# Performance work log

Measured on AMD Instinct MI355X. Metric: run time of the kernel, lower is better.

## Reference

```python
import jax, jax.numpy as jnp
import numpy as np

B, T, C, WE, H2 = 64, 256, 2048, 256, 1024  # batch, seq_len, num_classes, we_dim, 2*encoder_hidden_size


def setup_inputs() -> dict:
    key = jax.random.key(0)
    ks = jax.random.split(key, 8)
    s = 0.02
    encoder_outputs = jax.random.normal(ks[0], (B, T, H2), jnp.float32)
    words_num = jax.random.randint(ks[1], (B,), T // 2, T + 1)
    mask = jnp.arange(T)[None, :] < words_num[:, None]  # True = valid position
    targets = jax.random.randint(ks[2], (B, T), 0, C, dtype=jnp.int32)
    E = jax.random.normal(ks[3], (C, WE), jnp.float32) * s          # decoder token embedding
    W_ih = jax.random.normal(ks[4], (3 * H2, WE), jnp.float32) * s  # GRU input weights (r,z,n)
    W_hh = jax.random.normal(ks[5], (3 * H2, H2), jnp.float32) * s  # GRU hidden weights (r,z,n)
    b_ih = jnp.zeros((3 * H2,), jnp.float32)
    b_hh = jnp.zeros((3 * H2,), jnp.float32)
    W_out = jax.random.normal(ks[6], (C, 2 * H2), jnp.float32) * s  # Linear(4*enc_hidden -> C)
    b_out = jnp.zeros((C,), jnp.float32)
    return dict(encoder_outputs=encoder_outputs, mask=mask, targets=targets,
                E=E, W_ih=W_ih, W_hh=W_hh, b_ih=b_ih, b_hh=b_hh,
                W_out=W_out, b_out=b_out)


def reference(encoder_outputs, mask, targets, E, W_ih, W_hh, b_ih, b_hh, W_out, b_out):
    Bb, Tt, H = encoder_outputs.shape
    # Decoder hidden init: last encoder timestep (num_layers=1)
    h0 = encoder_outputs[:, -1, :]  # [B, H]
    # Teacher forcing: step-0 input is token id 0 (torch.zeros long), then targets[:, :-1]
    ids = jnp.concatenate([jnp.zeros((Bb, 1), targets.dtype), targets[:, :-1]], axis=1)
    x_seq = jnp.swapaxes(E[ids], 0, 1)  # [T, B, WE]
    # Precompute all GRU input projections in one GEMM: [T, B, 3H]
    gi = jnp.einsum('tbe,ge->tbg', x_seq, W_ih) + b_ih

    def step(h, gi_t):
        gh = h @ W_hh.T + b_hh                       # [B, 3H]
        ir, iz, inn = jnp.split(gi_t, 3, axis=-1)
        hr, hz, hn = jnp.split(gh, 3, axis=-1)
        r = jax.nn.sigmoid(ir + hr)
        z = jax.nn.sigmoid(iz + hz)
        n = jnp.tanh(inn + r * hn)
        h_new = (1.0 - z) * n + z * h                # GRU output == new hidden (1 step)
        # Luong dot attention: query = GRU output, keys = encoder outputs
        e = jnp.einsum('bh,bth->bt', h_new, encoder_outputs)
        e = jnp.where(mask, e, -jnp.inf)             # e[~valid] = -inf
        alpha = jax.nn.softmax(e, axis=-1)
        c = jnp.einsum('bt,bth->bh', alpha, encoder_outputs)
        logits = jnp.concatenate([h_new, c], axis=-1) @ W_out.T + b_out  # [B, C]
        return h_new, logits

    _, outs = jax.lax.scan(step, h0, gi)             # outs: [T, B, C]
    return jnp.swapaxes(outs, 0, 1)                  # [B, T, C]
```

## Files before the change

kernel.cpp:

```cpp
#include <hip/hip_runtime.h>
#include <hip/hip_bf16.h>
#include <math.h>

#define B_ 64
#define T_ 256
#define C_ 2048
#define WE_ 256
#define H_ 1024
#define G3_ 3072

typedef __attribute__((ext_vector_type(8))) short short8;
typedef __attribute__((ext_vector_type(4))) float f32x4;

__device__ __forceinline__ float sigmoidf_(float x) { return 1.f / (1.f + expf(-x)); }

__device__ __forceinline__ unsigned short f2bf(float v) {
    union { float f; unsigned int u; } x; x.f = v;
    unsigned int r = x.u + 0x7fffu + ((x.u >> 16) & 1u);
    return (unsigned short)(r >> 16);
}
__device__ __forceinline__ float bf2f(unsigned short h) {
    union { unsigned int u; float f; } x; x.u = ((unsigned int)h) << 16;
    return x.f;
}


__global__ void k_maskprep(const unsigned char* __restrict__ m, float* __restrict__ mf) {
    int idx = blockIdx.x * 256 + threadIdx.x;
    bool bytemode = (m[1] != 0);
    unsigned char v = bytemode ? m[idx] : m[(size_t)idx * 4];
    mf[idx] = v ? 1.f : 0.f;
}


__global__ void k_hinit2(const float* __restrict__ enc, float* __restrict__ h32,
                         unsigned short* __restrict__ h0h, unsigned short* __restrict__ h0l) {
    int idx = blockIdx.x * 256 + threadIdx.x;
    int b = idx >> 10, k = idx & (H_ - 1);
    float v = enc[((size_t)b * T_ + (T_ - 1)) * H_ + k];
    h32[idx] = v;
    unsigned short hi = f2bf(v);
    h0h[idx] = hi;
    h0l[idx] = f2bf(v - bf2f(hi));
}

__global__ void k_wgprep(const float* __restrict__ Wih, const float* __restrict__ Whh,
                         unsigned short* __restrict__ Wgh, unsigned short* __restrict__ Wgl) {
    int row = blockIdx.x;
    int c4 = threadIdx.x;
    int col = c4 * 4;
    float4 v = (col < 256) ? *(const float4*)&Wih[(size_t)row * 256 + col]
                           : *(const float4*)&Whh[(size_t)row * 1024 + col - 256];
    unsigned short h[4], l[4];
    float vv[4] = {v.x, v.y, v.z, v.w};
#pragma unroll
    for (int i = 0; i < 4; ++i) { h[i] = f2bf(vv[i]); l[i] = f2bf(vv[i] - bf2f(h[i])); }
    size_t o = (size_t)row * 1280 + col;
    *(uint2*)&Wgh[o] = *(const uint2*)h;
    *(uint2*)&Wgl[o] = *(const uint2*)l;
}

__global__ void k_xemb(const float* __restrict__ E, const int* __restrict__ targets,
                       unsigned short* __restrict__ Xeh, unsigned short* __restrict__ Xel) {
    int t = blockIdx.x, b = blockIdx.y, l = threadIdx.x;
    int id = (t == 0) ? 0 : targets[b * T_ + t - 1];
    float4 v = *(const float4*)&E[(size_t)id * 256 + l * 4];
    unsigned short h[4], lo[4];
    float vv[4] = {v.x, v.y, v.z, v.w};
#pragma unroll
    for (int i = 0; i < 4; ++i) { h[i] = f2bf(vv[i]); lo[i] = f2bf(vv[i] - bf2f(h[i])); }
    size_t o = (size_t)t * 16384 + (size_t)b * 256 + l * 4;
    *(uint2*)&Xeh[o] = *(const uint2*)h;
    *(uint2*)&Xel[o] = *(const uint2*)lo;
}

__global__ void k_encprep(const float* __restrict__ enc,
                          unsigned short* __restrict__ ench, unsigned short* __restrict__ encl) {
    size_t i4 = (size_t)blockIdx.x * 256 + threadIdx.x;
    float4 v = *(const float4*)&enc[i4 * 4];
    unsigned short h[4], l[4];
    float vv[4] = {v.x, v.y, v.z, v.w};
#pragma unroll
    for (int i = 0; i < 4; ++i) { h[i] = f2bf(vv[i]); l[i] = f2bf(vv[i] - bf2f(h[i])); }
    *(uint2*)&ench[i4 * 4] = *(const uint2*)h;
    *(uint2*)&encl[i4 * 4] = *(const uint2*)l;
}

__global__ __launch_bounds__(256) void k_step(
    const unsigned short* __restrict__ Xeh_t, const unsigned short* __restrict__ Xel_t,
    const unsigned short* __restrict__ Aph, const unsigned short* __restrict__ Apl, int ap_stride,
    const unsigned short* __restrict__ Wgh, const unsigned short* __restrict__ Wgl,
    const float* __restrict__ bih, const float* __restrict__ bhh,
    const float* __restrict__ h_prev32, float* __restrict__ h_next32,
    unsigned short* __restrict__ HhO, unsigned short* __restrict__ HlO)
{
    __shared__ unsigned short Ah[64 * 40], Al[64 * 40], Bh[48 * 40], Bl[48 * 40];
    __shared__ float bR[16], bZ[16], bNX[16], bNH[16];
    const int tid = threadIdx.x;
    const int j0 = blockIdx.x * 16;
    const int wave = tid >> 6, lane = tid & 63;
    const int ml = lane & 15, quad = lane >> 4;
    if (tid < 16) {
        int j = j0 + tid;
        bR[tid] = bih[j] + bhh[j];
        bZ[tid] = bih[1024 + j] + bhh[1024 + j];
        bNX[tid] = bih[2048 + j];
        bNH[tid] = bhh[2048 + j];
    }
    f32x4 accR = {0,0,0,0}, accZ = {0,0,0,0}, accNX = {0,0,0,0}, accNH = {0,0,0,0};
    const int ar = tid >> 2, aq = tid & 3;
    uint4 rAh = {0,0,0,0}, rAl = {0,0,0,0}, rBh = {0,0,0,0}, rBl = {0,0,0,0};
    {
        size_t off = (size_t)ar * 256 + aq * 8;
        rAh = *(const uint4*)&Xeh_t[off];
        rAl = *(const uint4*)&Xel_t[off];
    }
    if (tid < 192) {
        int g = ar >> 4, jj = ar & 15;
        size_t off = (size_t)(g * 1024 + j0 + jj) * 1280 + aq * 8;
        rBh = *(const uint4*)&Wgh[off];
        rBl = *(const uint4*)&Wgl[off];
    }
    for (int c = 0; c < 40; ++c) {
        *(uint4*)&Ah[ar * 40 + aq * 8] = rAh;
        *(uint4*)&Al[ar * 40 + aq * 8] = rAl;
        if (tid < 192) {
            *(uint4*)&Bh[ar * 40 + aq * 8] = rBh;
            *(uint4*)&Bl[ar * 40 + aq * 8] = rBl;
        }
        __syncthreads();
        if (c + 1 < 40) {
            int k0 = (c + 1) * 32;
            if (k0 < 256) {
                size_t off = (size_t)ar * 256 + k0 + aq * 8;
                rAh = *(const uint4*)&Xeh_t[off];
                rAl = *(const uint4*)&Xel_t[off];
            } else {
                size_t off = (size_t)ar * ap_stride + (k0 - 256) + aq * 8;
                rAh = *(const uint4*)&Aph[off];
                rAl = *(const uint4*)&Apl[off];
            }
            if (tid < 192) {
                int g = ar >> 4, jj = ar & 15;
                size_t off = (size_t)(g * 1024 + j0 + jj) * 1280 + k0 + aq * 8;
                rBh = *(const uint4*)&Wgh[off];
                rBl = *(const uint4*)&Wgl[off];
            }
        }
        short8 ah = *(const short8*)&Ah[(wave * 16 + ml) * 40 + quad * 8];
        short8 al = *(const short8*)&Al[(wave * 16 + ml) * 40 + quad * 8];
        short8 bh0 = *(const short8*)&Bh[(0 * 16 + ml) * 40 + quad * 8];
        short8 bl0 = *(const short8*)&Bl[(0 * 16 + ml) * 40 + quad * 8];
        short8 bh1 = *(const short8*)&Bh[(1 * 16 + ml) * 40 + quad * 8];
        short8 bl1 = *(const short8*)&Bl[(1 * 16 + ml) * 40 + quad * 8];
        short8 bh2 = *(const short8*)&Bh[(2 * 16 + ml) * 40 + quad * 8];
        short8 bl2 = *(const short8*)&Bl[(2 * 16 + ml) * 40 + quad * 8];
        accR = __builtin_amdgcn_mfma_f32_16x16x32_bf16(ah, bh0, accR, 0, 0, 0);
        accR = __builtin_amdgcn_mfma_f32_16x16x32_bf16(ah, bl0, accR, 0, 0, 0);
        accR = __builtin_amdgcn_mfma_f32_16x16x32_bf16(al, bh0, accR, 0, 0, 0);
        accZ = __builtin_amdgcn_mfma_f32_16x16x32_bf16(ah, bh1, accZ, 0, 0, 0);
        accZ = __builtin_amdgcn_mfma_f32_16x16x32_bf16(ah, bl1, accZ, 0, 0, 0);
        accZ = __builtin_amdgcn_mfma_f32_16x16x32_bf16(al, bh1, accZ, 0, 0, 0);
        if (c < 8) {
            accNX = __builtin_amdgcn_mfma_f32_16x16x32_bf16(ah, bh2, accNX, 0, 0, 0);
            accNX = __builtin_amdgcn_mfma_f32_16x16x32_bf16(ah, bl2, accNX, 0, 0, 0);
            accNX = __builtin_amdgcn_mfma_f32_16x16x32_bf16(al, bh2, accNX, 0, 0, 0);
        } else {
            accNH = __builtin_amdgcn_mfma_f32_16x16x32_bf16(ah, bh2, accNH, 0, 0, 0);
            accNH = __builtin_amdgcn_mfma_f32_16x16x32_bf16(ah, bl2, accNH, 0, 0, 0);
            accNH = __builtin_amdgcn_mfma_f32_16x16x32_bf16(al, bh2, accNH, 0, 0, 0);
        }
        __syncthreads();
    }
    int j = j0 + ml;
    float brv = bR[ml], bzv = bZ[ml], bnxv = bNX[ml], bnhv = bNH[ml];
#pragma unroll
    for (int reg = 0; reg < 4; ++reg) {
        int b = wave * 16 + quad * 4 + reg;
        float r = sigmoidf_(accR[reg] + brv);
        float z = sigmoidf_(accZ[reg] + bzv);
        float n = tanhf((accNX[reg] + bnxv) + r * (accNH[reg] + bnhv));
        float hp = h_prev32[(size_t)b * 1024 + j];
        float hv = (1.f - z) * n + z * hp;
        h_next32[(size_t)b * 1024 + j] = hv;
        unsigned short hi = f2bf(hv);
        HhO[(size_t)b * 262144 + j] = hi;
        HlO[(size_t)b * 262144 + j] = f2bf(hv - bf2f(hi));
    }
}

__global__ __launch_bounds__(256) void k_scoresK(
    const unsigned short* __restrict__ Hh, const unsigned short* __restrict__ Hl,
    const unsigned short* __restrict__ ench, const unsigned short* __restrict__ encl,
    float* __restrict__ e_all)
{
    __shared__ unsigned short Ahs[128 * 40], Als[128 * 40], Bhs[128 * 40], Bls[128 * 40];
    const int tid = threadIdx.x;
    const int b = blockIdx.y;
    const int t0 = (blockIdx.x & 1) * 128, p0 = (blockIdx.x >> 1) * 128;
    const int lane = tid & 63, wave = tid >> 6;
    const int wm = (wave & 1) * 64, wn = (wave >> 1) * 64;
    const int ml = lane & 15, quad = lane >> 4;
    const unsigned short* Ahp = Hh + (size_t)b * 262144;
    const unsigned short* Alp = Hl + (size_t)b * 262144;
    const unsigned short* Bhp = ench + (size_t)b * 262144;
    const unsigned short* Blp = encl + (size_t)b * 262144;
    f32x4 acc[4][4];
#pragma unroll
    for (int a = 0; a < 4; ++a)
#pragma unroll
        for (int c = 0; c < 4; ++c) acc[a][c] = (f32x4){0.f, 0.f, 0.f, 0.f};

    for (int kc = 0; kc < 32; ++kc) {
#pragma unroll
        for (int r2 = 0; r2 < 2; ++r2) {
            int s = tid + 256 * r2;
            int row = s >> 2, q = s & 3;
            size_t ga = (size_t)(t0 + row) * 1024 + kc * 32 + q * 8;
            size_t gb = (size_t)(p0 + row) * 1024 + kc * 32 + q * 8;
            *(uint4*)&Ahs[row * 40 + q * 8] = *(const uint4*)&Ahp[ga];
            *(uint4*)&Als[row * 40 + q * 8] = *(const uint4*)&Alp[ga];
            *(uint4*)&Bhs[row * 40 + q * 8] = *(const uint4*)&Bhp[gb];
            *(uint4*)&Bls[row * 40 + q * 8] = *(const uint4*)&Blp[gb];
        }
        __syncthreads();
        short8 ah[4], al[4], bh[4], bl[4];
#pragma unroll
        for (int mt = 0; mt < 4; ++mt) {
            ah[mt] = *(const short8*)&Ahs[(wm + mt * 16 + ml) * 40 + quad * 8];
            al[mt] = *(const short8*)&Als[(wm + mt * 16 + ml) * 40 + quad * 8];
        }
#pragma unroll
        for (int nt = 0; nt < 4; ++nt) {
            bh[nt] = *(const short8*)&Bhs[(wn + nt * 16 + ml) * 40 + quad * 8];
            bl[nt] = *(const short8*)&Bls[(wn + nt * 16 + ml) * 40 + quad * 8];
        }
#pragma unroll
        for (int mt = 0; mt < 4; ++mt)
#pragma unroll
            for (int nt = 0; nt < 4; ++nt) {
                acc[mt][nt] = __builtin_amdgcn_mfma_f32_16x16x32_bf16(ah[mt], bh[nt], acc[mt][nt], 0, 0, 0);
                acc[mt][nt] = __builtin_amdgcn_mfma_f32_16x16x32_bf16(ah[mt], bl[nt], acc[mt][nt], 0, 0, 0);
                acc[mt][nt] = __builtin_amdgcn_mfma_f32_16x16x32_bf16(al[mt], bh[nt], acc[mt][nt], 0, 0, 0);
            }
        __syncthreads();
    }
#pragma unroll
    for (int mt = 0; mt < 4; ++mt)
#pragma unroll
        for (int nt = 0; nt < 4; ++nt)
#pragma unroll
            for (int reg = 0; reg < 4; ++reg) {
                int t = t0 + wm + mt * 16 + quad * 4 + reg;
                int p = p0 + wn + nt * 16 + ml;
                e_all[((size_t)b * 256 + t) * 256 + p] = acc[mt][nt][reg];
            }
}

__global__ __launch_bounds__(256) void k_softmaxK(
    const float* __restrict__ e_all, const float* __restrict__ maskf,
    unsigned short* __restrict__ Ab)
{
    const int tid = threadIdx.x;
    const int ridx = blockIdx.x * 4 + (tid >> 6);
    const int lane = tid & 63;
    const int b = ridx >> 8, t = ridx & 255;
    const float* er = e_all + ((size_t)b * 256 + t) * 256;
    const float* mr = maskf + (size_t)b * 256;
    float v[4];
#pragma unroll
    for (int i = 0; i < 4; ++i) {
        int p = lane + 64 * i;
        v[i] = (mr[p] > 0.5f) ? er[p] : -INFINITY;
    }
    float m = fmaxf(fmaxf(v[0], v[1]), fmaxf(v[2], v[3]));
#pragma unroll
    for (int off = 32; off > 0; off >>= 1) m = fmaxf(m, __shfl_xor(m, off));
    float s = 0.f;
#pragma unroll
    for (int i = 0; i < 4; ++i) { v[i] = expf(v[i] - m); s += v[i]; }
#pragma unroll
    for (int off = 32; off > 0; off >>= 1) s += __shfl_xor(s, off);
    float inv = 1.f / s;
    unsigned short* arr = Ab + ((size_t)b * 256 + t) * 256;
#pragma unroll
    for (int i = 0; i < 4; ++i) arr[lane + 64 * i] = f2bf(v[i] * inv);
}

__global__ __launch_bounds__(256) void k_contextK(
    const unsigned short* __restrict__ Ab, const unsigned short* __restrict__ ench,
    unsigned short* __restrict__ Cb)
{
    __shared__ unsigned short As[128 * 40];
    __shared__ unsigned short Bs[128 * 40];
    const int tid = threadIdx.x;
    const int b = blockIdx.y;
    const int t0 = (blockIdx.x & 1) * 128;
    const int k0 = (blockIdx.x >> 1) * 128;
    const int lane = tid & 63, wave = tid >> 6;
    const int wm = (wave & 1) * 64, wn = (wave >> 1) * 64;
    const int ml = lane & 15, quad = lane >> 4;
    f32x4 acc[4][4];
#pragma unroll
    for (int a = 0; a < 4; ++a)
#pragma unroll
        for (int c = 0; c < 4; ++c) acc[a][c] = (f32x4){0.f, 0.f, 0.f, 0.f};

    for (int c = 0; c < 8; ++c) {
#pragma unroll
        for (int r2 = 0; r2 < 2; ++r2) {
            int s = tid + 256 * r2;
            int row = s >> 2, q = s & 3;
            *(uint4*)&As[row * 40 + q * 8] =
                *(const uint4*)&Ab[((size_t)b * 256 + t0 + row) * 256 + c * 32 + q * 8];
        }
        {
            int tr = tid >> 3, kq = tid & 7;
            const unsigned short* src =
                ench + ((size_t)b * 256 + c * 32 + tr) * 1024 + k0 + kq * 16;
            unsigned short tmp[16];
            *(uint4*)&tmp[0] = *(const uint4*)&src[0];
            *(uint4*)&tmp[8] = *(const uint4*)&src[8];
#pragma unroll
            for (int i = 0; i < 16; ++i)
                Bs[(kq * 16 + i) * 40 + tr] = tmp[i];
        }
        __syncthreads();
        short8 af[4], bf[4];
#pragma unroll
        for (int mt = 0; mt < 4; ++mt)
            af[mt] = *(const short8*)&As[(wm + mt * 16 + ml) * 40 + quad * 8];
#pragma unroll
        for (int nt = 0; nt < 4; ++nt)
            bf[nt] = *(const short8*)&Bs[(wn + nt * 16 + ml) * 40 + quad * 8];
#pragma unroll
        for (int mt = 0; mt < 4; ++mt)
#pragma unroll
            for (int nt = 0; nt < 4; ++nt)
                acc[mt][nt] = __builtin_amdgcn_mfma_f32_16x16x32_bf16(af[mt], bf[nt], acc[mt][nt], 0, 0, 0);
        __syncthreads();
    }
#pragma unroll
    for (int mt = 0; mt < 4; ++mt)
#pragma unroll
        for (int nt = 0; nt < 4; ++nt)
#pragma unroll
            for (int reg = 0; reg < 4; ++reg) {
                int t = t0 + wm + mt * 16 + quad * 4 + reg;
                int k = k0 + wn + nt * 16 + ml;
                Cb[((size_t)b * 256 + t) * 1024 + k] = f2bf(acc[mt][nt][reg]);
            }
}

__global__ __launch_bounds__(256) void k_finalK(
    const unsigned short* __restrict__ Hh, const unsigned short* __restrict__ Cb,
    const unsigned short* __restrict__ Wb,
    const float* __restrict__ bout, float* __restrict__ out)
{
    __shared__ unsigned short As[128 * 40];
    __shared__ unsigned short Bs[128 * 40];
    const int tid = threadIdx.x;
    const int gr0 = blockIdx.x * 128;
    const int j0  = blockIdx.y * 128;
    const int lane = tid & 63, wave = tid >> 6;
    const int wm = (wave & 1) * 64, wn = (wave >> 1) * 64;
    const int ml = lane & 15, quad = lane >> 4;
    f32x4 acc[4][4];
#pragma unroll
    for (int a = 0; a < 4; ++a)
#pragma unroll
        for (int c = 0; c < 4; ++c) acc[a][c] = (f32x4){0.f, 0.f, 0.f, 0.f};

    for (int kc = 0; kc < 64; ++kc) {
        const unsigned short* asrc = (kc < 32) ? Hh : Cb;
        int ko = (kc & 31) * 32;
#pragma unroll
        for (int r2 = 0; r2 < 2; ++r2) {
            int s = tid + 256 * r2;
            int row = s >> 2, q = s & 3;
            *(uint4*)&As[row * 40 + q * 8] =
                *(const uint4*)&asrc[(size_t)(gr0 + row) * 1024 + ko + q * 8];
            *(uint4*)&Bs[row * 40 + q * 8] =
                *(const uint4*)&Wb[(size_t)(j0 + row) * 2048 + kc * 32 + q * 8];
        }
        __syncthreads();
        short8 af[4], bf[4];
#pragma unroll
        for (int mt = 0; mt < 4; ++mt)
            af[mt] = *(const short8*)&As[(wm + mt * 16 + ml) * 40 + quad * 8];
#pragma unroll
        for (int nt = 0; nt < 4; ++nt)
            bf[nt] = *(const short8*)&Bs[(wn + nt * 16 + ml) * 40 + quad * 8];
#pragma unroll
        for (int mt = 0; mt < 4; ++mt)
#pragma unroll
            for (int nt = 0; nt < 4; ++nt)
                acc[mt][nt] = __builtin_amdgcn_mfma_f32_16x16x32_bf16(af[mt], bf[nt], acc[mt][nt], 0, 0, 0);
        __syncthreads();
    }
#pragma unroll
    for (int nt = 0; nt < 4; ++nt) {
        int j = j0 + wn + nt * 16 + ml;
        float bo = bout[j];
#pragma unroll
        for (int mt = 0; mt < 4; ++mt)
#pragma unroll
            for (int reg = 0; reg < 4; ++reg) {
                int r = gr0 + wm + mt * 16 + quad * 4 + reg;
                out[(size_t)r * 2048 + j] = acc[mt][nt][reg] + bo;
            }
    }
}


__global__ void k_hinit(const float* __restrict__ enc, float* __restrict__ h) {
    int idx = blockIdx.x * 256 + threadIdx.x;
    int b = idx >> 10, k = idx & (H_ - 1);
    h[idx] = enc[((size_t)b * T_ + (T_ - 1)) * H_ + k];
}

__global__ void k_wprep(const float* __restrict__ Wout, __hip_bfloat16* __restrict__ Wb) {
    int i4 = blockIdx.x * 256 + threadIdx.x;
    float4 v = *(const float4*)&Wout[(size_t)i4 * 4];
    __attribute__((aligned(8))) __hip_bfloat16 tmp[4] = {
        __float2bfloat16(v.x), __float2bfloat16(v.y),
        __float2bfloat16(v.z), __float2bfloat16(v.w)};
    *(uint2*)&Wb[(size_t)i4 * 4] = *(const uint2*)tmp;
}

__global__ __launch_bounds__(256) void k_gates(
    const float* __restrict__ E, const int* __restrict__ targets,
    const float* __restrict__ Wih, const float* __restrict__ Whh,
    const float* __restrict__ bih, const float* __restrict__ bhh,
    const float* __restrict__ h_cur,
    float* __restrict__ gi, float* __restrict__ gh0, float* __restrict__ gh1,
    int t)
{
    __shared__ float As[32 * 68];
    __shared__ float Ws[32 * 34];
    __shared__ int ids[B_];
    const int tid = threadIdx.x;
    const int z = blockIdx.y;
    const int j0 = blockIdx.x * 32;
    const int tx = tid & 15;
    const int ty = tid >> 4;
    float accI[4][2], accH[4][2];
#pragma unroll
    for (int i = 0; i < 4; ++i) { accI[i][0]=0.f; accI[i][1]=0.f; accH[i][0]=0.f; accH[i][1]=0.f; }
    if (tid < B_) ids[tid] = (t == 0) ? 0 : targets[tid * T_ + t - 1];
    __syncthreads();
    if (z == 0) {
        for (int c = 0; c < 8; ++c) {
            int k0 = c * 32;
#pragma unroll
            for (int r = 0; r < 2; ++r) {
                int lin = tid + 256 * r;
                int k4 = lin & 7, b = lin >> 3;
                float4 v = *(const float4*)&E[(size_t)ids[b] * WE_ + k0 + k4 * 4];
                int kk = k4 * 4;
                As[(kk + 0) * 68 + b] = v.x; As[(kk + 1) * 68 + b] = v.y;
                As[(kk + 2) * 68 + b] = v.z; As[(kk + 3) * 68 + b] = v.w;
            }
            {
                int k4 = tid & 7, jj = tid >> 3;
                float4 v = *(const float4*)&Wih[(size_t)(j0 + jj) * WE_ + k0 + k4 * 4];
                int kk = k4 * 4;
                Ws[(kk + 0) * 34 + jj] = v.x; Ws[(kk + 1) * 34 + jj] = v.y;
                Ws[(kk + 2) * 34 + jj] = v.z; Ws[(kk + 3) * 34 + jj] = v.w;
            }
            __syncthreads();
#pragma unroll
            for (int kk = 0; kk < 32; ++kk) {
                float4 a = *(const float4*)&As[kk * 68 + ty * 4];
                float2 w = *(const float2*)&Ws[kk * 34 + tx * 2];
                accI[0][0] += a.x * w.x; accI[0][1] += a.x * w.y;
                accI[1][0] += a.y * w.x; accI[1][1] += a.y * w.y;
                accI[2][0] += a.z * w.x; accI[2][1] += a.z * w.y;
                accI[3][0] += a.w * w.x; accI[3][1] += a.w * w.y;
            }
            __syncthreads();
        }
    }
    const int c_lo = (z == 0) ? 0 : 12;
    const int c_hi = (z == 0) ? 12 : 32;
    for (int c = c_lo; c < c_hi; ++c) {
        int k0 = c * 32;
#pragma unroll
        for (int r = 0; r < 2; ++r) {
            int lin = tid + 256 * r;
            int k4 = lin & 7, b = lin >> 3;
            float4 v = *(const float4*)&h_cur[(size_t)b * H_ + k0 + k4 * 4];
            int kk = k4 * 4;
            As[(kk + 0) * 68 + b] = v.x; As[(kk + 1) * 68 + b] = v.y;
            As[(kk + 2) * 68 + b] = v.z; As[(kk + 3) * 68 + b] = v.w;
        }
        {
            int k4 = tid & 7, jj = tid >> 3;
            float4 v = *(const float4*)&Whh[(size_t)(j0 + jj) * H_ + k0 + k4 * 4];
            int kk = k4 * 4;
            Ws[(kk + 0) * 34 + jj] = v.x; Ws[(kk + 1) * 34 + jj] = v.y;
            Ws[(kk + 2) * 34 + jj] = v.z; Ws[(kk + 3) * 34 + jj] = v.w;
        }
        __syncthreads();
#pragma unroll
        for (int kk = 0; kk < 32; ++kk) {
            float4 a = *(const float4*)&As[kk * 68 + ty * 4];
            float2 w = *(const float2*)&Ws[kk * 34 + tx * 2];
            accH[0][0] += a.x * w.x; accH[0][1] += a.x * w.y;
            accH[1][0] += a.y * w.x; accH[1][1] += a.y * w.y;
            accH[2][0] += a.z * w.x; accH[2][1] += a.z * w.y;
            accH[3][0] += a.w * w.x; accH[3][1] += a.w * w.y;
        }
        __syncthreads();
    }
#pragma unroll
    for (int p = 0; p < 2; ++p) {
        int j = j0 + tx * 2 + p;
        if (z == 0) {
            float vi = bih[j], vh = bhh[j];
#pragma unroll
            for (int i = 0; i < 4; ++i) {
                int b = ty * 4 + i;
                gi[(size_t)b * G3_ + j]  = accI[i][p] + vi;
                gh0[(size_t)b * G3_ + j] = accH[i][p] + vh;
            }
        } else {
#pragma unroll
            for (int i = 0; i < 4; ++i) {
                int b = ty * 4 + i;
                gh1[(size_t)b * G3_ + j] = accH[i][p];
            }
        }
    }
}

__global__ __launch_bounds__(256) void k_score_h(
    const float* __restrict__ gi, const float* __restrict__ gh0, const float* __restrict__ gh1,
    const float* __restrict__ h_prev, const float* __restrict__ enc,
    float* __restrict__ e_raw, float* __restrict__ h_next,
    __hip_bfloat16* __restrict__ Xb, int t, int use_x)
{
    __shared__ float hs[H_];
    const int b = blockIdx.y;
    const int tc = blockIdx.x;
    const int tid = threadIdx.x;
#pragma unroll
    for (int i = 0; i < 4; ++i) {
        int k = i * 256 + tid;
        size_t o = (size_t)b * G3_ + k;
        float ir = gi[o], iz = gi[o + H_], in = gi[o + 2 * H_];
        float hr = gh0[o] + gh1[o];
        float hz = gh0[o + H_] + gh1[o + H_];
        float hn = gh0[o + 2 * H_] + gh1[o + 2 * H_];
        float r = sigmoidf_(ir + hr);
        float z = sigmoidf_(iz + hz);
        float n = tanhf(in + r * hn);
        float hv = (1.f - z) * n + z * h_prev[(size_t)b * H_ + k];
        hs[k] = hv;
        if (tc == 0) {
            h_next[(size_t)b * H_ + k] = hv;
            if (use_x) Xb[((size_t)b * T_ + t) * C_ + k] = __float2bfloat16(hv);
        }
    }
    __syncthreads();
    const int tl = tid >> 2, part = tid & 3;
    const int tt = tc * 64 + tl;
    const float4* row = (const float4*)(enc + ((size_t)b * T_ + tt) * H_);
    const float4* hv4 = (const float4*)hs;
    float acc = 0.f;
#pragma unroll 8
    for (int i = 0; i < 64; ++i) {
        float4 a = row[part * 64 + i];
        float4 x = hv4[part * 64 + i];
        acc += a.x * x.x + a.y * x.y + a.z * x.z + a.w * x.w;
    }
    acc += __shfl_xor(acc, 1);
    acc += __shfl_xor(acc, 2);
    if (part == 0) e_raw[(size_t)b * T_ + tt] = acc;
}

__global__ __launch_bounds__(256) void k_ctx(
    const float* __restrict__ e_raw, const float* __restrict__ maskf,
    const float* __restrict__ enc, float* __restrict__ cvec,
    __hip_bfloat16* __restrict__ Xb, int t, int use_x)
{
    __shared__ float al[T_];
    __shared__ float red[256];
    const int b = blockIdx.y, q = blockIdx.x, tid = threadIdx.x;
    float e = (maskf[(size_t)b * T_ + tid] > 0.5f) ? e_raw[(size_t)b * T_ + tid] : -INFINITY;
    red[tid] = e; __syncthreads();
    for (int s = 128; s > 0; s >>= 1) { if (tid < s) red[tid] = fmaxf(red[tid], red[tid + s]); __syncthreads(); }
    float mx = red[0]; __syncthreads();
    float p = expf(e - mx);
    red[tid] = p; __syncthreads();
    for (int s = 128; s > 0; s >>= 1) { if (tid < s) red[tid] += red[tid + s]; __syncthreads(); }
    float denom = red[0];
    al[tid] = p / denom;
    __syncthreads();
    const int k = q * 256 + tid;
    float acc = 0.f;
#pragma unroll 8
    for (int tt2 = 0; tt2 < T_; ++tt2) {
        acc += al[tt2] * enc[((size_t)b * T_ + tt2) * H_ + k];
    }
    if (use_x) Xb[((size_t)b * T_ + t) * C_ + H_ + k] = __float2bfloat16(acc);
    else       cvec[(size_t)b * H_ + k] = acc;
}

__global__ __launch_bounds__(256) void k_logits(
    const float* __restrict__ h, const float* __restrict__ cvec,
    const float* __restrict__ Wout, const float* __restrict__ bout,
    float* __restrict__ out, int t)
{
    __shared__ float As[32 * 68];
    __shared__ float Ws[32 * 33];
    const int tid = threadIdx.x;
    const int j0 = blockIdx.x * 32;
    const int tx = tid & 31;
    const int ty = tid >> 5;
    float acc[8];
#pragma unroll
    for (int i = 0; i < 8; ++i) acc[i] = 0.f;
    for (int c = 0; c < 64; ++c) {
        int k0 = c * 32;
        const float* Ap = (k0 < H_) ? (h + k0) : (cvec + (k0 - H_));
#pragma unroll
        for (int r = 0; r < 2; ++r) {
            int lin = tid + 256 * r;
            int k4 = lin & 7, b = lin >> 3;
            float4 v = *(const float4*)&Ap[(size_t)b * H_ + k4 * 4];
            int kk = k4 * 4;
            As[(kk + 0) * 68 + b] = v.x; As[(kk + 1) * 68 + b] = v.y;
            As[(kk + 2) * 68 + b] = v.z; As[(kk + 3) * 68 + b] = v.w;
        }
        {
            int k4 = tid & 7, jj = tid >> 3;
            float4 v = *(const float4*)&Wout[(size_t)(j0 + jj) * (2 * H_) + k0 + k4 * 4];
            int kk = k4 * 4;
            Ws[(kk + 0) * 33 + jj] = v.x; Ws[(kk + 1) * 33 + jj] = v.y;
            Ws[(kk + 2) * 33 + jj] = v.z; Ws[(kk + 3) * 33 + jj] = v.w;
        }
        __syncthreads();
#pragma unroll
        for (int kk = 0; kk < 32; ++kk) {
            float w = Ws[kk * 33 + tx];
#pragma unroll
            for (int i = 0; i < 8; ++i) acc[i] += As[kk * 68 + ty * 8 + i] * w;
        }
        __syncthreads();
    }
    float bo = bout[j0 + tx];
#pragma unroll
    for (int i = 0; i < 8; ++i) {
        int b = ty * 8 + i;
        out[((size_t)b * T_ + t) * C_ + j0 + tx] = acc[i] + bo;
    }
}

__global__ __launch_bounds__(256) void k_final(
    const __hip_bfloat16* __restrict__ Xb, const __hip_bfloat16* __restrict__ Wb,
    const float* __restrict__ bout, float* __restrict__ out)
{
    __shared__ __hip_bfloat16 As[128 * 40];
    __shared__ __hip_bfloat16 Bs[128 * 40];
    const int tid = threadIdx.x;
    const int gr0 = blockIdx.x * 128;
    const int j0  = blockIdx.y * 128;
    const int lane = tid & 63, wave = tid >> 6;
    const int wm = (wave & 1) * 64, wn = (wave >> 1) * 64;
    const int ml = lane & 15, quad = lane >> 4;
    f32x4 acc[4][4];
#pragma unroll
    for (int a = 0; a < 4; ++a)
#pragma unroll
        for (int b = 0; b < 4; ++b) acc[a][b] = (f32x4){0.f, 0.f, 0.f, 0.f};
    for (int kc = 0; kc < 64; ++kc) {
#pragma unroll
        for (int r = 0; r < 2; ++r) {
            int s = tid + 256 * r;
            int row = s >> 2, kq = s & 3;
            *(uint4*)&As[row * 40 + kq * 8] =
                *(const uint4*)&Xb[(size_t)(gr0 + row) * 2048 + kc * 32 + kq * 8];
            *(uint4*)&Bs[row * 40 + kq * 8] =
                *(const uint4*)&Wb[(size_t)(j0 + row) * 2048 + kc * 32 + kq * 8];
        }
        __syncthreads();
        short8 af[4], bf[4];
#pragma unroll
        for (int mt = 0; mt < 4; ++mt)
            af[mt] = *(const short8*)&As[(wm + mt * 16 + ml) * 40 + quad * 8];
#pragma unroll
        for (int nt = 0; nt < 4; ++nt)
            bf[nt] = *(const short8*)&Bs[(wn + nt * 16 + ml) * 40 + quad * 8];
#pragma unroll
        for (int mt = 0; mt < 4; ++mt)
#pragma unroll
            for (int nt = 0; nt < 4; ++nt)
                acc[mt][nt] = __builtin_amdgcn_mfma_f32_16x16x32_bf16(af[mt], bf[nt], acc[mt][nt], 0, 0, 0);
        __syncthreads();
    }
#pragma unroll
    for (int nt = 0; nt < 4; ++nt) {
        int j = j0 + wn + nt * 16 + ml;
        float bo = bout[j];
#pragma unroll
        for (int mt = 0; mt < 4; ++mt) {
#pragma unroll
            for (int reg = 0; reg < 4; ++reg) {
                int r = gr0 + wm + mt * 16 + quad * 4 + reg;
                out[(size_t)r * 2048 + j] = acc[mt][nt][reg] + bo;
            }
        }
    }
}


extern "C" void kernel_launch(void* const* d_in, const int* in_sizes, int n_in,
                              void* d_out, int out_size, void* d_ws, size_t ws_size,
                              hipStream_t stream)
{
    const float* enc     = (const float*)d_in[0];
    const unsigned char* mask = (const unsigned char*)d_in[1];
    const int*   targets = (const int*)d_in[2];
    const float* E       = (const float*)d_in[3];
    const float* Wih     = (const float*)d_in[4];
    const float* Whh     = (const float*)d_in[5];
    const float* bih     = (const float*)d_in[6];
    const float* bhh     = (const float*)d_in[7];
    const float* Wout    = (const float*)d_in[8];
    const float* bout    = (const float*)d_in[9];
    float* out = (float*)d_out;

    const size_t NEED_FULL = 235000000ull;
    const size_t NEED_MID  = 819200ull * 4 + (4194304ull + 33554432ull) * 2;

    if (ws_size >= NEED_FULL) {
        char* p = (char*)d_ws;
        float* h32a = (float*)p;              p += 262144;
        float* h32b = (float*)p;              p += 262144;
        unsigned short* h0h = (unsigned short*)p; p += 131072;
        unsigned short* h0l = (unsigned short*)p; p += 131072;
        float* maskf = (float*)p;             p += 65536;
        unsigned short* Wgh = (unsigned short*)p; p += 7864320;
        unsigned short* Wgl = (unsigned short*)p; p += 7864320;
        unsigned short* Xeh = (unsigned short*)p; p += 8388608;
        unsigned short* Xel = (unsigned short*)p; p += 8388608;
        unsigned short* ench = (unsigned short*)p; p += 33554432;
        unsigned short* encl = (unsigned short*)p; p += 33554432;
        unsigned short* Hh = (unsigned short*)p;  p += 33554432;
        unsigned short* Hl = (unsigned short*)p;  p += 33554432;
        float* e_all = (float*)p;             p += 16777216;
        unsigned short* Ab = (unsigned short*)p;  p += 8388608;
        unsigned short* Cb = (unsigned short*)p;  p += 33554432;
        unsigned short* Wb = (unsigned short*)p;  p += 8388608;

        k_maskprep<<<64, 256, 0, stream>>>(mask, maskf);
        k_hinit2<<<256, 256, 0, stream>>>(enc, h32a, h0h, h0l);
        k_wgprep<<<3072, 320, 0, stream>>>(Wih, Whh, Wgh, Wgl);
        k_xemb<<<dim3(256, 64), 64, 0, stream>>>(E, targets, Xeh, Xel);
        k_encprep<<<16384, 256, 0, stream>>>(enc, ench, encl);
        k_wprep<<<4096, 256, 0, stream>>>(Wout, (__hip_bfloat16*)Wb);

        for (int t = 0; t < T_; ++t) {
            const unsigned short* Xeh_t = Xeh + (size_t)t * 16384;
            const unsigned short* Xel_t = Xel + (size_t)t * 16384;
            const unsigned short* Aph = (t == 0) ? h0h : (Hh + (size_t)(t - 1) * 1024);
            const unsigned short* Apl = (t == 0) ? h0l : (Hl + (size_t)(t - 1) * 1024);
            int ap_stride = (t == 0) ? 1024 : 262144;
            const float* hp = (t & 1) ? h32b : h32a;
            float* hn = (t & 1) ? h32a : h32b;
            k_step<<<64, 256, 0, stream>>>(Xeh_t, Xel_t, Aph, Apl, ap_stride,
                                           Wgh, Wgl, bih, bhh, hp, hn,
                                           Hh + (size_t)t * 1024, Hl + (size_t)t * 1024);
        }
        k_scoresK<<<dim3(4, 64), 256, 0, stream>>>(Hh, Hl, ench, encl, e_all);
        k_softmaxK<<<4096, 256, 0, stream>>>(e_all, maskf, Ab);
        k_contextK<<<dim3(16, 64), 256, 0, stream>>>(Ab, ench, Cb);
        k_finalK<<<dim3(128, 16), 256, 0, stream>>>(Hh, Cb, Wb, bout, out);
        return;
    }

    float* ws    = (float*)d_ws;
    float* hbuf  = ws;
    float* gi    = ws + 131072;
    float* gh0   = gi + 196608;
    float* gh1   = gh0 + 196608;
    float* e_raw = gh1 + 196608;
    float* maskf = e_raw + 16384;
    float* cvec  = maskf + 16384;
    __hip_bfloat16* Wb = (__hip_bfloat16*)(ws + 819200);
    __hip_bfloat16* Xb = Wb + 4194304;

    const int fast = (ws_size >= NEED_MID) ? 1 : 0;

    k_maskprep<<<64, 256, 0, stream>>>(mask, maskf);
    k_hinit<<<256, 256, 0, stream>>>(enc, hbuf);
    if (fast) k_wprep<<<4096, 256, 0, stream>>>(Wout, Wb);

    for (int t = 0; t < T_; ++t) {
        float* h_cur  = hbuf + (t & 1) * 65536;
        float* h_next = hbuf + ((t + 1) & 1) * 65536;
        k_gates<<<dim3(96, 2), 256, 0, stream>>>(E, targets, Wih, Whh, bih, bhh,
                                                 h_cur, gi, gh0, gh1, t);
        k_score_h<<<dim3(4, 64), 256, 0, stream>>>(gi, gh0, gh1, h_cur, enc,
                                                   e_raw, h_next, Xb, t, fast);
        k_ctx<<<dim3(4, 64), 256, 0, stream>>>(e_raw, maskf, enc, cvec, Xb, t, fast);
        if (!fast)
            k_logits<<<64, 256, 0, stream>>>(h_next, cvec, Wout, bout, out, t);
    }
    if (fast)
        k_final<<<dim3(128, 16), 256, 0, stream>>>(Xb, Wb, bout, out);
}
```

Baseline: 6.162 ms.

## Replace per-timestep GRU launches with persistent kernel using grid-wide barrier

Swaps the 256 per-step k_step launches for a single persistent k_rnn kernel of 128 blocks. The blocks synchronize through a global atomic counter barrier, and split-K partial sums pass between paired blocks via flags and a global scratch buffer. Weights are read straight from global memory (L2) into registers with software prefetch instead of being staged through LDS. This removes launch overhead and per-step LDS staging, at the cost of spin-wait barriers. It also relies on all 128 blocks being co-resident, or the barrier will deadlock.

```diff
diff --git a/kernel.cpp b/kernel.cpp
--- a/kernel.cpp
+++ b/kernel.cpp
@@ -24,6 +24,12 @@
     return x.f;
 }
 
+#define LD8(p, off) (*(const short8*)((p) + (off)))
+
+
+__global__ void k_zero(unsigned int* __restrict__ p) {
+    p[blockIdx.x * 256 + threadIdx.x] = 0u;
+}
 
 __global__ void k_maskprep(const unsigned char* __restrict__ m, float* __restrict__ mf) {
     int idx = blockIdx.x * 256 + threadIdx.x;
@@ -32,16 +38,14 @@
     mf[idx] = v ? 1.f : 0.f;
 }
 
-
-__global__ void k_hinit2(const float* __restrict__ enc, float* __restrict__ h32,
-                         unsigned short* __restrict__ h0h, unsigned short* __restrict__ h0l) {
+__global__ void k_hinit0(const float* __restrict__ enc,
+                         unsigned short* __restrict__ Hh, unsigned short* __restrict__ Hl) {
     int idx = blockIdx.x * 256 + threadIdx.x;
-    int b = idx >> 10, k = idx & (H_ - 1);
+    int b = idx >> 10, k = idx & 1023;
     float v = enc[((size_t)b * T_ + (T_ - 1)) * H_ + k];
-    h32[idx] = v;
     unsigned short hi = f2bf(v);
-    h0h[idx] = hi;
-    h0l[idx] = f2bf(v - bf2f(hi));
+    Hh[idx] = hi;
+    Hl[idx] = f2bf(v - bf2f(hi));
 }
 
 __global__ void k_wgprep(const float* __restrict__ Wih, const float* __restrict__ Whh,
@@ -86,108 +90,167 @@
     *(uint2*)&encl[i4 * 4] = *(const uint2*)l;
 }
 
-__global__ __launch_bounds__(256) void k_step(
-    const unsigned short* __restrict__ Xeh_t, const unsigned short* __restrict__ Xel_t,
-    const unsigned short* __restrict__ Aph, const unsigned short* __restrict__ Apl, int ap_stride,
+__global__ void k_wprep(const float* __restrict__ Wout, unsigned short* __restrict__ Wb) {
+    int i4 = blockIdx.x * 256 + threadIdx.x;
+    float4 v = *(const float4*)&Wout[(size_t)i4 * 4];
+    unsigned short t[4] = {f2bf(v.x), f2bf(v.y), f2bf(v.z), f2bf(v.w)};
+    *(uint2*)&Wb[(size_t)i4 * 4] = *(const uint2*)t;
+}
+
+__global__ __launch_bounds__(512, 2) void k_rnn(
+    const unsigned short* __restrict__ Xeh, const unsigned short* __restrict__ Xel,
     const unsigned short* __restrict__ Wgh, const unsigned short* __restrict__ Wgl,
     const float* __restrict__ bih, const float* __restrict__ bhh,
-    const float* __restrict__ h_prev32, float* __restrict__ h_next32,
-    unsigned short* __restrict__ HhO, unsigned short* __restrict__ HlO)
-{
-    __shared__ unsigned short Ah[64 * 40], Al[64 * 40], Bh[48 * 40], Bl[48 * 40];
-    __shared__ float bR[16], bZ[16], bNX[16], bNH[16];
+    unsigned short* __restrict__ Hh, unsigned short* __restrict__ Hl,
+    float* __restrict__ gpart, unsigned int* __restrict__ flags,
+    unsigned int* __restrict__ barcnt)
+{
+    __shared__ float red[3072];
     const int tid = threadIdx.x;
-    const int j0 = blockIdx.x * 16;
     const int wave = tid >> 6, lane = tid & 63;
     const int ml = lane & 15, quad = lane >> 4;
-    if (tid < 16) {
-        int j = j0 + tid;
-        bR[tid] = bih[j] + bhh[j];
-        bZ[tid] = bih[1024 + j] + bhh[1024 + j];
-        bNX[tid] = bih[2048 + j];
-        bNH[tid] = bhh[2048 + j];
-    }
-    f32x4 accR = {0,0,0,0}, accZ = {0,0,0,0}, accNX = {0,0,0,0}, accNH = {0,0,0,0};
-    const int ar = tid >> 2, aq = tid & 3;
-    uint4 rAh = {0,0,0,0}, rAl = {0,0,0,0}, rBh = {0,0,0,0}, rBl = {0,0,0,0};
-    {
-        size_t off = (size_t)ar * 256 + aq * 8;
-        rAh = *(const uint4*)&Xeh_t[off];
-        rAl = *(const uint4*)&Xel_t[off];
-    }
-    if (tid < 192) {
-        int g = ar >> 4, jj = ar & 15;
-        size_t off = (size_t)(g * 1024 + j0 + jj) * 1280 + aq * 8;
-        rBh = *(const uint4*)&Wgh[off];
-        rBl = *(const uint4*)&Wgl[off];
-    }
-    for (int c = 0; c < 40; ++c) {
-        *(uint4*)&Ah[ar * 40 + aq * 8] = rAh;
-        *(uint4*)&Al[ar * 40 + aq * 8] = rAl;
-        if (tid < 192) {
-            *(uint4*)&Bh[ar * 40 + aq * 8] = rBh;
-            *(uint4*)&Bl[ar * 40 + aq * 8] = rBl;
-        }
-        __syncthreads();
-        if (c + 1 < 40) {
-            int k0 = (c + 1) * 32;
-            if (k0 < 256) {
-                size_t off = (size_t)ar * 256 + k0 + aq * 8;
-                rAh = *(const uint4*)&Xeh_t[off];
-                rAl = *(const uint4*)&Xel_t[off];
+    const int mw = wave & 3, ksub = wave >> 2;
+    const int triple = blockIdx.x >> 1, kh = blockIdx.x & 1;
+    const int j0 = triple * 16;
+    const int m0 = mw * 16;
+    const int kbase = kh * 640 + ksub * 320;
+
+    float bRv = 0.f, bZv = 0.f, bNXv = 0.f, bNHv = 0.f;
+    if (kh == 0 && ksub == 0) {
+        int j = j0 + ml;
+        bRv = bih[j] + bhh[j];
+        bZv = bih[1024 + j] + bhh[1024 + j];
+        bNXv = bih[2048 + j];
+        bNHv = bhh[2048 + j];
+    }
+
+    const size_t bo = (size_t)(j0 + ml) * 1280 + quad * 8;
+    const unsigned short* BrH = Wgh + bo;
+    const unsigned short* BrL = Wgl + bo;
+    const unsigned short* BzH = Wgh + bo + (size_t)1024 * 1280;
+    const unsigned short* BzL = Wgl + bo + (size_t)1024 * 1280;
+    const unsigned short* BnH = Wgh + bo + (size_t)2048 * 1280;
+    const unsigned short* BnL = Wgl + bo + (size_t)2048 * 1280;
+
+    const unsigned short* AxH = Xeh + (size_t)(m0 + ml) * 256 + quad * 8;
+    const unsigned short* AxL = Xel + (size_t)(m0 + ml) * 256 + quad * 8;
+    const unsigned short* AhH = Hh + (size_t)(m0 + ml) * 1024 + quad * 8 - 256;
+    const unsigned short* AhL = Hl + (size_t)(m0 + ml) * 1024 + quad * 8 - 256;
+    const unsigned short* Hh_t = Hh;
+    const unsigned short* Hl_t = Hl;
+
+    for (int t = 0; t < 256; ++t) {
+        f32x4 aR = {0,0,0,0}, aZ = {0,0,0,0}, aNX = {0,0,0,0}, aNH = {0,0,0,0};
+        short8 cah, cal, cb0h, cb0l, cb1h, cb1l, cb2h, cb2l;
+        {
+            int k0 = kbase;
+            if (k0 < 256) { cah = LD8(AxH, k0); cal = LD8(AxL, k0); }
+            else          { cah = LD8(AhH, k0); cal = LD8(AhL, k0); }
+            cb0h = LD8(BrH, k0); cb0l = LD8(BrL, k0);
+            cb1h = LD8(BzH, k0); cb1l = LD8(BzL, k0);
+            cb2h = LD8(BnH, k0); cb2l = LD8(BnL, k0);
+        }
+#pragma unroll
+        for (int c = 0; c < 10; ++c) {
+            short8 nah, nal, nb0h, nb0l, nb1h, nb1l, nb2h, nb2l;
+            if (c < 9) {
+                int k0n = kbase + (c + 1) * 32;
+                if (k0n < 256) { nah = LD8(AxH, k0n); nal = LD8(AxL, k0n); }
+                else           { nah = LD8(AhH, k0n); nal = LD8(AhL, k0n); }
+                nb0h = LD8(BrH, k0n); nb0l = LD8(BrL, k0n);
+                nb1h = LD8(BzH, k0n); nb1l = LD8(BzL, k0n);
+                nb2h = LD8(BnH, k0n); nb2l = LD8(BnL, k0n);
+            }
+            aR = __builtin_amdgcn_mfma_f32_16x16x32_bf16(cah, cb0h, aR, 0, 0, 0);
+            aR = __builtin_amdgcn_mfma_f32_16x16x32_bf16(cah, cb0l, aR, 0, 0, 0);
+            aR = __builtin_amdgcn_mfma_f32_16x16x32_bf16(cal, cb0h, aR, 0, 0, 0);
+            aZ = __builtin_amdgcn_mfma_f32_16x16x32_bf16(cah, cb1h, aZ, 0, 0, 0);
+            aZ = __builtin_amdgcn_mfma_f32_16x16x32_bf16(cah, cb1l, aZ, 0, 0, 0);
+            aZ = __builtin_amdgcn_mfma_f32_16x16x32_bf16(cal, cb1h, aZ, 0, 0, 0);
+            if (kbase + c * 32 < 256) {
+                aNX = __builtin_amdgcn_mfma_f32_16x16x32_bf16(cah, cb2h, aNX, 0, 0, 0);
+                aNX = __builtin_amdgcn_mfma_f32_16x16x32_bf16(cah, cb2l, aNX, 0, 0, 0);
+                aNX = __builtin_amdgcn_mfma_f32_16x16x32_bf16(cal, cb2h, aNX, 0, 0, 0);
             } else {
-                size_t off = (size_t)ar * ap_stride + (k0 - 256) + aq * 8;
-                rAh = *(const uint4*)&Aph[off];
-                rAl = *(const uint4*)&Apl[off];
-            }
-            if (tid < 192) {
-                int g = ar >> 4, jj = ar & 15;
-                size_t off = (size_t)(g * 1024 + j0 + jj) * 1280 + k0 + aq * 8;
-                rBh = *(const uint4*)&Wgh[off];
-                rBl = *(const uint4*)&Wgl[off];
-            }
-        }
-        short8 ah = *(const short8*)&Ah[(wave * 16 + ml) * 40 + quad * 8];
-        short8 al = *(const short8*)&Al[(wave * 16 + ml) * 40 + quad * 8];
-        short8 bh0 = *(const short8*)&Bh[(0 * 16 + ml) * 40 + quad * 8];
-        short8 bl0 = *(const short8*)&Bl[(0 * 16 + ml) * 40 + quad * 8];
-        short8 bh1 = *(const short8*)&Bh[(1 * 16 + ml) * 40 + quad * 8];
-        short8 bl1 = *(const short8*)&Bl[(1 * 16 + ml) * 40 + quad * 8];
-        short8 bh2 = *(const short8*)&Bh[(2 * 16 + ml) * 40 + quad * 8];
-        short8 bl2 = *(const short8*)&Bl[(2 * 16 + ml) * 40 + quad * 8];
-        accR = __builtin_amdgcn_mfma_f32_16x16x32_bf16(ah, bh0, accR, 0, 0, 0);
-        accR = __builtin_amdgcn_mfma_f32_16x16x32_bf16(ah, bl0, accR, 0, 0, 0);
-        accR = __builtin_amdgcn_mfma_f32_16x16x32_bf16(al, bh0, accR, 0, 0, 0);
-        accZ = __builtin_amdgcn_mfma_f32_16x16x32_bf16(ah, bh1, accZ, 0, 0, 0);
-        accZ = __builtin_amdgcn_mfma_f32_16x16x32_bf16(ah, bl1, accZ, 0, 0, 0);
-        accZ = __builtin_amdgcn_mfma_f32_16x16x32_bf16(al, bh1, accZ, 0, 0, 0);
-        if (c < 8) {
-            accNX = __builtin_amdgcn_mfma_f32_16x16x32_bf16(ah, bh2, accNX, 0, 0, 0);
-            accNX = __builtin_amdgcn_mfma_f32_16x16x32_bf16(ah, bl2, accNX, 0, 0, 0);
-            accNX = __builtin_amdgcn_mfma_f32_16x16x32_bf16(al, bh2, accNX, 0, 0, 0);
+                aNH = __builtin_amdgcn_mfma_f32_16x16x32_bf16(cah, cb2h, aNH, 0, 0, 0);
+                aNH = __builtin_amdgcn_mfma_f32_16x16x32_bf16(cah, cb2l, aNH, 0, 0, 0);
+                aNH = __builtin_amdgcn_mfma_f32_16x16x32_bf16(cal, cb2h, aNH, 0, 0, 0);
+            }
+            if (c < 9) {
+                cah = nah; cal = nal;
+                cb0h = nb0h; cb0l = nb0l;
+                cb1h = nb1h; cb1l = nb1l;
+                cb2h = nb2h; cb2l = nb2l;
+            }
+        }
+        if (ksub == 1) {
+            *(f32x4*)&red[((mw * 3 + 0) * 64 + lane) * 4] = aR;
+            *(f32x4*)&red[((mw * 3 + 1) * 64 + lane) * 4] = aZ;
+            *(f32x4*)&red[((mw * 3 + 2) * 64 + lane) * 4] = aNH;
+        }
+        __syncthreads();
+        if (ksub == 0) {
+            aR  += *(const f32x4*)&red[((mw * 3 + 0) * 64 + lane) * 4];
+            aZ  += *(const f32x4*)&red[((mw * 3 + 1) * 64 + lane) * 4];
+            aNH += *(const f32x4*)&red[((mw * 3 + 2) * 64 + lane) * 4];
+        }
+        if (kh == 1) {
+            if (ksub == 0) {
+#pragma unroll
+                for (int reg = 0; reg < 4; ++reg) {
+                    int b = m0 + quad * 4 + reg;
+                    gpart[((triple * 3 + 0) * 64 + b) * 16 + ml] = aR[reg];
+                    gpart[((triple * 3 + 1) * 64 + b) * 16 + ml] = aZ[reg];
+                    gpart[((triple * 3 + 2) * 64 + b) * 16 + ml] = aNH[reg];
+                }
+                __threadfence();
+            }
+            __syncthreads();
+            if (tid == 0)
+                __hip_atomic_store(&flags[t * 64 + triple], 1u,
+                                   __ATOMIC_RELEASE, __HIP_MEMORY_SCOPE_AGENT);
         } else {
-            accNH = __builtin_amdgcn_mfma_f32_16x16x32_bf16(ah, bh2, accNH, 0, 0, 0);
-            accNH = __builtin_amdgcn_mfma_f32_16x16x32_bf16(ah, bl2, accNH, 0, 0, 0);
-            accNH = __builtin_amdgcn_mfma_f32_16x16x32_bf16(al, bh2, accNH, 0, 0, 0);
-        }
-        __syncthreads();
-    }
-    int j = j0 + ml;
-    float brv = bR[ml], bzv = bZ[ml], bnxv = bNX[ml], bnhv = bNH[ml];
-#pragma unroll
-    for (int reg = 0; reg < 4; ++reg) {
-        int b = wave * 16 + quad * 4 + reg;
-        float r = sigmoidf_(accR[reg] + brv);
-        float z = sigmoidf_(accZ[reg] + bzv);
-        float n = tanhf((accNX[reg] + bnxv) + r * (accNH[reg] + bnhv));
-        float hp = h_prev32[(size_t)b * 1024 + j];
-        float hv = (1.f - z) * n + z * hp;
-        h_next32[(size_t)b * 1024 + j] = hv;
-        unsigned short hi = f2bf(hv);
-        HhO[(size_t)b * 262144 + j] = hi;
-        HlO[(size_t)b * 262144 + j] = f2bf(hv - bf2f(hi));
-    }
-}
+            if (tid == 0) {
+                while (__hip_atomic_load(&flags[t * 64 + triple],
+                                         __ATOMIC_ACQUIRE, __HIP_MEMORY_SCOPE_AGENT) == 0u)
+                    __builtin_amdgcn_s_sleep(1);
+            }
+            __syncthreads();
+            if (ksub == 0) {
+                int j = j0 + ml;
+                size_t slotN = (size_t)(t + 1) * 65536;
+#pragma unroll
+                for (int reg = 0; reg < 4; ++reg) {
+                    int b = m0 + quad * 4 + reg;
+                    float R  = aR[reg]  + gpart[((triple * 3 + 0) * 64 + b) * 16 + ml] + bRv;
+                    float Z  = aZ[reg]  + gpart[((triple * 3 + 1) * 64 + b) * 16 + ml] + bZv;
+                    float NH = aNH[reg] + gpart[((triple * 3 + 2) * 64 + b) * 16 + ml] + bNHv;
+                    float rr = sigmoidf_(R), zz = sigmoidf_(Z);
+                    float nn = tanhf(aNX[reg] + bNXv + rr * NH);
+                    size_t po = (size_t)b * 1024 + j;
+                    float hp = bf2f(Hh_t[po]) + bf2f(Hl_t[po]);
+                    float hv = (1.f - zz) * nn + zz * hp;
+                    unsigned short hi = f2bf(hv);
+                    Hh[slotN + po] = hi;
+                    Hl[slotN + po] = f2bf(hv - bf2f(hi));
+                }
+                __threadfence();
+            }
+        }
+        __syncthreads();
+        if (tid == 0) {
+            __hip_atomic_fetch_add(barcnt, 1u, __ATOMIC_RELEASE, __HIP_MEMORY_SCOPE_AGENT);
+            unsigned int target = 128u * (unsigned int)(t + 1);
+            while (__hip_atomic_load(barcnt, __ATOMIC_ACQUIRE, __HIP_MEMORY_SCOPE_AGENT) < target)
+                __builtin_amdgcn_s_sleep(2);
+        }
+        __syncthreads();
+        AxH += 16384; AxL += 16384;
+        AhH += 65536; AhL += 65536;
+        Hh_t += 65536; Hl_t += 65536;
+    }
+}
+
 
 __global__ __launch_bounds__(256) void k_scoresK(
     const unsigned short* __restrict__ Hh, const unsigned short* __restrict__ Hl,
@@ -201,10 +264,6 @@
     const int lane = tid & 63, wave = tid >> 6;
     const int wm = (wave & 1) * 64, wn = (wave >> 1) * 64;
     const int ml = lane & 15, quad = lane >> 4;
-    const unsigned short* Ahp = Hh + (size_t)b * 262144;
-    const unsigned short* Alp = Hl + (size_t)b * 262144;
-    const unsigned short* Bhp = ench + (size_t)b * 262144;
-    const unsigned short* Blp = encl + (size_t)b * 262144;
     f32x4 acc[4][4];
 #pragma unroll
     for (int a = 0; a < 4; ++a)
@@ -216,12 +275,12 @@
         for (int r2 = 0; r2 < 2; ++r2) {
             int s = tid + 256 * r2;
             int row = s >> 2, q = s & 3;
-            size_t ga = (size_t)(t0 + row) * 1024 + kc * 32 + q * 8;
-            size_t gb = (size_t)(p0 + row) * 1024 + kc * 32 + q * 8;
-            *(uint4*)&Ahs[row * 40 + q * 8] = *(const uint4*)&Ahp[ga];
-            *(uint4*)&Als[row * 40 + q * 8] = *(const uint4*)&Alp[ga];
-            *(uint4*)&Bhs[row * 40 + q * 8] = *(const uint4*)&Bhp[gb];
-            *(uint4*)&Bls[row * 40 + q * 8] = *(const uint4*)&Blp[gb];
+            size_t ga = ((size_t)(t0 + row + 1) * 64 + b) * 1024 + kc * 32 + q * 8;
+            size_t gb = ((size_t)b * 256 + p0 + row) * 1024 + kc * 32 + q * 8;
+            *(uint4*)&Ahs[row * 40 + q * 8] = *(const uint4*)&Hh[ga];
+            *(uint4*)&Als[row * 40 + q * 8] = *(const uint4*)&Hl[ga];
+            *(uint4*)&Bhs[row * 40 + q * 8] = *(const uint4*)&ench[gb];
+            *(uint4*)&Bls[row * 40 + q * 8] = *(const uint4*)&encl[gb];
         }
         __syncthreads();
         short8 ah[4], al[4], bh[4], bl[4];
@@ -372,14 +431,17 @@
         for (int c = 0; c < 4; ++c) acc[a][c] = (f32x4){0.f, 0.f, 0.f, 0.f};
 
     for (int kc = 0; kc < 64; ++kc) {
-        const unsigned short* asrc = (kc < 32) ? Hh : Cb;
         int ko = (kc & 31) * 32;
 #pragma unroll
         for (int r2 = 0; r2 < 2; ++r2) {
             int s = tid + 256 * r2;
             int row = s >> 2, q = s & 3;
-            *(uint4*)&As[row * 40 + q * 8] =
-                *(const uint4*)&asrc[(size_t)(gr0 + row) * 1024 + ko + q * 8];
+            int r0 = gr0 + row;
+            size_t ga;
+            if (kc < 32) ga = ((size_t)((r0 & 255) + 1) * 64 + (r0 >> 8)) * 1024 + ko + q * 8;
+            else         ga = (size_t)r0 * 1024 + ko + q * 8;
+            const unsigned short* asrc = (kc < 32) ? Hh : Cb;
+            *(uint4*)&As[row * 40 + q * 8] = *(const uint4*)&asrc[ga];
             *(uint4*)&Bs[row * 40 + q * 8] =
                 *(const uint4*)&Wb[(size_t)(j0 + row) * 2048 + kc * 32 + q * 8];
         }
@@ -417,15 +479,6 @@
     int idx = blockIdx.x * 256 + threadIdx.x;
     int b = idx >> 10, k = idx & (H_ - 1);
     h[idx] = enc[((size_t)b * T_ + (T_ - 1)) * H_ + k];
-}
-
-__global__ void k_wprep(const float* __restrict__ Wout, __hip_bfloat16* __restrict__ Wb) {
-    int i4 = blockIdx.x * 256 + threadIdx.x;
-    float4 v = *(const float4*)&Wout[(size_t)i4 * 4];
-    __attribute__((aligned(8))) __hip_bfloat16 tmp[4] = {
-        __float2bfloat16(v.x), __float2bfloat16(v.y),
-        __float2bfloat16(v.z), __float2bfloat16(v.w)};
-    *(uint2*)&Wb[(size_t)i4 * 4] = *(const uint2*)tmp;
 }
 
 __global__ __launch_bounds__(256) void k_gates(
@@ -731,48 +784,40 @@
     const float* bout    = (const float*)d_in[9];
     float* out = (float*)d_out;
 
-    const size_t NEED_FULL = 235000000ull;
+    const size_t NEED_FULL = 218300416ull;
     const size_t NEED_MID  = 819200ull * 4 + (4194304ull + 33554432ull) * 2;
 
     if (ws_size >= NEED_FULL) {
         char* p = (char*)d_ws;
-        float* h32a = (float*)p;              p += 262144;
-        float* h32b = (float*)p;              p += 262144;
-        unsigned short* h0h = (unsigned short*)p; p += 131072;
-        unsigned short* h0l = (unsigned short*)p; p += 131072;
-        float* maskf = (float*)p;             p += 65536;
+        unsigned int* flags = (unsigned int*)p;
+        unsigned int* barcnt = flags + 16384;
+        p += 131072;
+        float* maskf = (float*)p;                p += 65536;
         unsigned short* Wgh = (unsigned short*)p; p += 7864320;
         unsigned short* Wgl = (unsigned short*)p; p += 7864320;
         unsigned short* Xeh = (unsigned short*)p; p += 8388608;
         unsigned short* Xel = (unsigned short*)p; p += 8388608;
+        float* e_all = (float*)Xeh;
         unsigned short* ench = (unsigned short*)p; p += 33554432;
         unsigned short* encl = (unsigned short*)p; p += 33554432;
-        unsigned short* Hh = (unsigned short*)p;  p += 33554432;
-        unsigned short* Hl = (unsigned short*)p;  p += 33554432;
-        float* e_all = (float*)p;             p += 16777216;
+        unsigned short* Hh = (unsigned short*)p;  p += 33685504;
+        unsigned short* Hl = (unsigned short*)p;  p += 33685504;
         unsigned short* Ab = (unsigned short*)p;  p += 8388608;
         unsigned short* Cb = (unsigned short*)p;  p += 33554432;
         unsigned short* Wb = (unsigned short*)p;  p += 8388608;
-
+        float* gpart = (float*)p;                 p += 786432;
+
+        k_zero<<<128, 256, 0, stream>>>(flags);
         k_maskprep<<<64, 256, 0, stream>>>(mask, maskf);
-        k_hinit2<<<256, 256, 0, stream>>>(enc, h32a, h0h, h0l);
+        k_hinit0<<<256, 256, 0, stream>>>(enc, Hh, Hl);
         k_wgprep<<<3072, 320, 0, stream>>>(Wih, Whh, Wgh, Wgl);
         k_xemb<<<dim3(256, 64), 64, 0, stream>>>(E, targets, Xeh, Xel);
         k_encprep<<<16384, 256, 0, stream>>>(enc, ench, encl);
-        k_wprep<<<4096, 256, 0, stream>>>(Wout, (__hip_bfloat16*)Wb);
-
-        for (int t = 0; t < T_; ++t) {
-            const unsigned short* Xeh_t = Xeh + (size_t)t * 16384;
-            const unsigned short* Xel_t = Xel + (size_t)t * 16384;
-            const unsigned short* Aph = (t == 0) ? h0h : (Hh + (size_t)(t - 1) * 1024);
-            const unsigned short* Apl = (t == 0) ? h0l : (Hl + (size_t)(t - 1) * 1024);
-            int ap_stride = (t == 0) ? 1024 : 262144;
-            const float* hp = (t & 1) ? h32b : h32a;
-            float* hn = (t & 1) ? h32a : h32b;
-            k_step<<<64, 256, 0, stream>>>(Xeh_t, Xel_t, Aph, Apl, ap_stride,
-                                           Wgh, Wgl, bih, bhh, hp, hn,
-                                           Hh + (size_t)t * 1024, Hl + (size_t)t * 1024);
-        }
+        k_wprep<<<4096, 256, 0, stream>>>(Wout, Wb);
+
+        k_rnn<<<128, 512, 0, stream>>>(Xeh, Xel, Wgh, Wgl, bih, bhh,
+                                       Hh, Hl, gpart, flags, barcnt);
+
         k_scoresK<<<dim3(4, 64), 256, 0, stream>>>(Hh, Hl, ench, encl, e_all);
         k_softmaxK<<<4096, 256, 0, stream>>>(e_all, maskf, Ab);
         k_contextK<<<dim3(16, 64), 256, 0, stream>>>(Ab, ench, Cb);
@@ -795,7 +840,7 @@
 
     k_maskprep<<<64, 256, 0, stream>>>(mask, maskf);
     k_hinit<<<256, 256, 0, stream>>>(enc, hbuf);
-    if (fast) k_wprep<<<4096, 256, 0, stream>>>(Wout, Wb);
+    if (fast) k_wprep<<<4096, 256, 0, stream>>>(Wout, (unsigned short*)Wb);
 
     for (int t = 0; t < T_; ++t) {
         float* h_cur  = hbuf + (t & 1) * 65536;
```

Result: slower. 12.59 ms (+104.3%).
